# Optimization experiments

Hardware: AMD Instinct MI355X
Metric: run time of the kernel (lower is better)

Reference implementation:

```python
import jax, jax.numpy as jnp
import numpy as np

P, N, F, H, D_HID = 3, 4096, 1024, 8, 8
EMBED = H * D_HID  # 64
ATT, C = 128, 16


def setup_inputs() -> dict:
    key = jax.random.key(0)
    ks = jax.random.split(key, 12)
    return {
        "inputs": jax.random.normal(ks[0], (P, N, F), jnp.float32),
        # bias_mat plays the role of an additive adjacency mask; random floats are fine for math checking
        "bias_mat": jax.random.normal(ks[1], (P, N, N), jnp.float32),
        "W": jax.random.normal(ks[2], (P, H, F, D_HID), jnp.float32) * 0.05,
        "a1_w": jax.random.normal(ks[3], (P, H, D_HID), jnp.float32) * 0.1,
        "a1_b": jax.random.normal(ks[4], (P, H), jnp.float32) * 0.1,
        "a2_w": jax.random.normal(ks[5], (P, H, D_HID), jnp.float32) * 0.1,
        "a2_b": jax.random.normal(ks[6], (P, H), jnp.float32) * 0.1,
        "h_bias": jnp.zeros((P, H, D_HID), jnp.float32),
        "Ws": jax.random.normal(ks[7], (EMBED, ATT), jnp.float32) * 0.1,
        "bs": jax.random.normal(ks[8], (ATT,), jnp.float32) * 0.1,
        "u": jax.random.normal(ks[9], (ATT,), jnp.float32) * 0.1,
        "Wc": jax.random.normal(ks[10], (EMBED, C), jnp.float32) * 0.05,
        "bc": jnp.zeros((C,), jnp.float32),
    }


def reference(inputs, bias_mat, W, a1_w, a1_b, a2_w, a2_b, h_bias, Ws, bs, u, Wc, bc):
    # inputs: [P,N,F], bias_mat: [P,N,N]
    embeds = []
    for p in range(inputs.shape[0]):  # small fixed loop over meta-paths
        seq = inputs[p]                                            # [N,F]
        fts = jnp.einsum('nf,hfd->hnd', seq, W[p])                 # shared projection, all heads
        f1 = jnp.einsum('hnd,hd->hn', fts, a1_w[p]) + a1_b[p][:, None]
        f2 = jnp.einsum('hnd,hd->hn', fts, a2_w[p]) + a2_b[p][:, None]
        logits = f1[:, :, None] + f2[:, None, :]                   # [H,N,N] additive attention
        coefs = jax.nn.softmax(jax.nn.leaky_relu(logits) + bias_mat[p][None], axis=-1)
        vals = jnp.einsum('hnm,hmd->hnd', coefs, fts) + h_bias[p][:, None, :]
        h = jax.nn.elu(vals)                                       # activation per head
        embeds.append(jnp.transpose(h, (1, 0, 2)).reshape(h.shape[1], -1))  # concat heads -> [N,H*d]
    multi = jnp.stack(embeds, axis=1)                              # [N,P,EMBED]
    # semantic (meta-path) attention
    v = jnp.tanh(multi @ Ws + bs)                                  # [N,P,ATT]
    alphas = jax.nn.softmax(v @ u, axis=-1)                        # [N,P]
    final = jnp.sum(multi * alphas[:, :, None], axis=1)            # [N,EMBED]
    # single final classifier head (mean over 1 head == identity)
    logits_out = final @ Wc + bc                                   # [N,C]
    return logits_out, final, alphas
```

## Files before the change

### kernel.cpp

```cpp
#include <hip/hip_runtime.h>

#define LOG2E 1.44269504088896f

typedef _Float16 f16;
typedef _Float16 f16x8 __attribute__((ext_vector_type(8)));
typedef float f32x4 __attribute__((ext_vector_type(4)));

#define NP 3
#define NN 4096
#define FF 1024
#define HH 8
#define DD 8
#define HD 64

#define OFF_F1S   0
#define OFF_F2S   393216
#define OFF_F2MAX 589824
#define OFF_FTST  590080
#define OFF_MULTI 2162944

#define OUT_FINAL 65536
#define OUT_ALPHA 327680

__global__ __launch_bounds__(256) void kA(const float* __restrict__ inp,
                                          const float* __restrict__ W,
                                          const float* __restrict__ a1w,
                                          const float* __restrict__ a1b,
                                          const float* __restrict__ a2w,
                                          const float* __restrict__ a2b,
                                          char* __restrict__ ws) {
    __shared__ float At[32 * 68];
    __shared__ float Bt[32 * 64];
    __shared__ float ftile[64 * 68];
    const int tid = threadIdx.x;
    const int p = blockIdx.y;
    const int n0 = blockIdx.x * 64;

    const int tr = tid >> 4, tc = tid & 15;
    const int r0 = tr * 4, c0 = tc * 4;
    const int sr = tid >> 2, sq = tid & 3;
    const int bc = tid & 63, bkq = tid >> 6;
    const int hB = bc >> 3, dB = bc & 7;

    float acc[4][4] = {};

    for (int kb = 0; kb < 32; ++kb) {
        const float* asrc = inp + ((size_t)p * NN + n0 + sr) * FF + kb * 32 + sq * 8;
        float4 v0 = *(const float4*)asrc;
        float4 v1 = *(const float4*)(asrc + 4);
        int kbase = sq * 8;
        At[(kbase + 0) * 68 + sr] = v0.x; At[(kbase + 1) * 68 + sr] = v0.y;
        At[(kbase + 2) * 68 + sr] = v0.z; At[(kbase + 3) * 68 + sr] = v0.w;
        At[(kbase + 4) * 68 + sr] = v1.x; At[(kbase + 5) * 68 + sr] = v1.y;
        At[(kbase + 6) * 68 + sr] = v1.z; At[(kbase + 7) * 68 + sr] = v1.w;
        #pragma unroll
        for (int i = 0; i < 8; ++i) {
            int k = bkq * 8 + i;
            Bt[k * 64 + bc] = W[(((size_t)p * HH + hB) * FF + kb * 32 + k) * DD + dB];
        }
        __syncthreads();
        #pragma unroll
        for (int k = 0; k < 32; ++k) {
            float4 av = *(const float4*)&At[k * 68 + r0];
            float4 bv = *(const float4*)&Bt[k * 64 + c0];
            float aa[4] = {av.x, av.y, av.z, av.w};
            float bb[4] = {bv.x, bv.y, bv.z, bv.w};
            #pragma unroll
            for (int i = 0; i < 4; ++i)
                #pragma unroll
                for (int j = 0; j < 4; ++j) acc[i][j] += aa[i] * bb[j];
        }
        __syncthreads();
    }
    #pragma unroll
    for (int i = 0; i < 4; ++i) {
        float4 o;
        o.x = acc[i][0]; o.y = acc[i][1]; o.z = acc[i][2]; o.w = acc[i][3];
        *(float4*)&ftile[(r0 + i) * 68 + c0] = o;
    }
    __syncthreads();

    float* f1s = (float*)(ws + OFF_F1S);
    f16* f2s = (f16*)(ws + OFF_F2S);
    #pragma unroll
    for (int rep = 0; rep < 2; ++rep) {
        int task = tid + rep * 256;
        int row = task >> 3, h = task & 7;
        const float* fb = &ftile[row * 68 + h * 8];
        float s1 = a1b[p * HH + h], s2 = a2b[p * HH + h];
        #pragma unroll
        for (int d = 0; d < 8; ++d) {
            float v = fb[d];
            s1 += v * a1w[((size_t)p * HH + h) * DD + d];
            s2 += v * a2w[((size_t)p * HH + h) * DD + d];
        }
        f1s[((size_t)p * HH + h) * NN + n0 + row] = s1 * LOG2E;
        f2s[((size_t)p * HH + h) * NN + n0 + row] = (f16)(s2 * LOG2E);
    }
    {
        f16* ftsT = (f16*)(ws + OFF_FTST);
        int cc2 = tid >> 2, rq = (tid & 3) * 16;
        union { f16 h[16]; uint4 u[2]; } pk;
        #pragma unroll
        for (int i = 0; i < 16; ++i) pk.h[i] = (f16)ftile[(rq + i) * 68 + cc2];
        uint4* dst = (uint4*)(ftsT + ((size_t)p * HD + cc2) * NN + n0 + rq);
        dst[0] = pk.u[0];
        dst[1] = pk.u[1];
    }
}

__global__ __launch_bounds__(64) void kA2(char* __restrict__ ws) {
    const f16* f2s = (const f16*)(ws + OFF_F2S);
    float* fmax = (float*)(ws + OFF_F2MAX);
    int b = blockIdx.x;
    int lane = threadIdx.x;
    float v = -1e30f;
    for (int m = lane; m < NN; m += 64) v = fmaxf(v, (float)f2s[(size_t)b * NN + m]);
    #pragma unroll
    for (int off = 32; off >= 1; off >>= 1) v = fmaxf(v, __shfl_xor(v, off, 64));
    if (lane == 0) fmax[b] = v;
}

__global__ __launch_bounds__(256) void kB(const float* __restrict__ bias,
                                          const float* __restrict__ h_bias,
                                          char* __restrict__ ws) {
    __shared__ __align__(16) char smem[38544];
    f16* ftsL = (f16*)smem;
    f16* f2L = (f16*)(smem + 34320);

    const int tid = threadIdx.x;
    const int lane = tid & 63, wv = tid >> 6;
    const int c = lane & 15, kg = lane >> 4;
    const int p = blockIdx.y;
    const int n0 = blockIdx.x * 16;
    const int n = n0 + c;

    const float* f1s = (const float*)(ws + OFF_F1S);
    const f16* f2s = (const f16*)(ws + OFF_F2S);
    const float* fmax = (const float*)(ws + OFF_F2MAX);
    const f16* ftsG = (const f16*)(ws + OFF_FTST);
    float* multi = (float*)(ws + OFF_MULTI);

    float f18[8], ub[8];
    #pragma unroll
    for (int h = 0; h < 8; ++h) {
        float f1v = f1s[((size_t)p * 8 + h) * NN + n];
        float fm = fmax[p * 8 + h];
        float x = f1v + fm;
        float lr = fmaxf(x, 0.01f * x);
        ub[h] = lr + 8.0f * LOG2E;
        f18[h] = f1v;
    }
    f32x4 acc[8] = {};

    for (int i = tid; i < 264; i += 256) ftsL[64 * 264 + i] = (f16)1.0f;

    const int scc = tid >> 2, sq = tid & 3;
    const int fh = (tid & 127) >> 4, fq = tid & 15;

    for (int ch = 0; ch < 16; ++ch) {
        int m0 = ch * 256;
        {
            const uint4* src = (const uint4*)(ftsG + ((size_t)p * HD + scc) * NN + m0 + sq * 64);
            uint4* dst = (uint4*)(ftsL + scc * 264 + sq * 64);
            #pragma unroll
            for (int i = 0; i < 8; ++i) dst[i] = src[i];
        }
        if (tid < 128) {
            const uint4* src = (const uint4*)(f2s + ((size_t)p * 8 + fh) * NN + m0 + fq * 16);
            uint4* dst = (uint4*)(f2L + fh * 264 + fq * 16);
            dst[0] = src[0];
            dst[1] = src[1];
        }
        __syncthreads();
        #pragma unroll
        for (int s = 0; s < 2; ++s) {
            int mloc = wv * 64 + s * 32 + kg * 8;
            const float* bp = bias + ((size_t)p * NN + n) * NN + m0 + mloc;
            float4 b0 = *(const float4*)bp;
            float4 b1 = *(const float4*)(bp + 4);
            float bb[8] = {b0.x, b0.y, b0.z, b0.w, b1.x, b1.y, b1.z, b1.w};
            #pragma unroll
            for (int h = 0; h < 8; ++h) {
                f16x8 f2v = *(const f16x8*)(f2L + h * 264 + mloc);
                int rB = (c < 8) ? (h * 8 + c) : 64;
                f16x8 bf = *(const f16x8*)(ftsL + rB * 264 + mloc);
                union { f16x8 v; f16 e[8]; } af;
                #pragma unroll
                for (int j = 0; j < 8; ++j) {
                    float x = f18[h] + (float)f2v[j];
                    float lr = fmaxf(x, 0.01f * x);
                    float e = __builtin_amdgcn_exp2f(fmaf(bb[j], LOG2E, lr - ub[h]));
                    af.e[j] = (f16)e;
                }
                acc[h] = __builtin_amdgcn_mfma_f32_16x16x32_f16(af.v, bf, acc[h], 0, 0, 0);
            }
        }
        __syncthreads();
    }

    float* red = (float*)smem;
    #pragma unroll
    for (int h = 0; h < 8; ++h) {
        if (c <= 8) {
            #pragma unroll
            for (int r = 0; r < 4; ++r)
                red[((wv * 8 + h) * 16 + kg * 4 + r) * 9 + c] = acc[h][r];
        }
    }
    __syncthreads();
    #pragma unroll
    for (int rep = 0; rep < 4; ++rep) {
        int idx = tid + rep * 256;
        int R = idx >> 6, hd = idx & 63;
        int h = hd >> 3, d = hd & 7;
        float v = 0.f, l = 0.f;
        #pragma unroll
        for (int w = 0; w < 4; ++w) {
            v += red[((w * 8 + h) * 16 + R) * 9 + d];
            l += red[((w * 8 + h) * 16 + R) * 9 + 8];
        }
        float o = v / l + h_bias[(p * 8 + h) * 8 + d];
        o = o > 0.f ? o : (__builtin_amdgcn_exp2f(o * LOG2E) - 1.0f);
        multi[((size_t)(n0 + R) * NP + p) * HD + hd] = o;
    }
}

__global__ __launch_bounds__(256) void kC(const float* __restrict__ Ws,
                                          const float* __restrict__ bsv,
                                          const float* __restrict__ uv,
                                          const float* __restrict__ Wc,
                                          const float* __restrict__ bcv,
                                          char* __restrict__ ws,
                                          float* __restrict__ out) {
    __shared__ float WsL[64 * 128];
    __shared__ float mult[16 * 3 * 64];
    __shared__ float WcL[64 * 16];
    __shared__ float uL[128], bsL[128], bcL[16];
    __shared__ float vred[16 * 3 * 16];
    __shared__ float alphaL[16 * 3];
    __shared__ float fin[16 * 64];
    const int tid = threadIdx.x;
    const int n0 = blockIdx.x * 16;
    const float* multi = (const float*)(ws + OFF_MULTI);

    for (int i = tid; i < 64 * 128; i += 256) WsL[i] = Ws[i];
    for (int i = tid; i < 3072; i += 256) mult[i] = multi[(size_t)n0 * 192 + i];
    for (int i = tid; i < 1024; i += 256) WcL[i] = Wc[i];
    if (tid < 128) { uL[tid] = uv[tid]; bsL[tid] = bsv[tid]; }
    if (tid < 16) bcL[tid] = bcv[tid];
    __syncthreads();

    const int nl = tid >> 4, j = tid & 15;
    for (int p = 0; p < 3; ++p) {
        float va[8] = {};
        for (int e = 0; e < 64; ++e) {
            float me = mult[(nl * 3 + p) * 64 + e];
            #pragma unroll
            for (int i = 0; i < 8; ++i) va[i] += me * WsL[e * 128 + j + 16 * i];
        }
        float part = 0.f;
        #pragma unroll
        for (int i = 0; i < 8; ++i) part += tanhf(va[i] + bsL[j + 16 * i]) * uL[j + 16 * i];
        vred[(nl * 3 + p) * 16 + j] = part;
    }
    __syncthreads();
    if (tid < 16) {
        float sc[3];
        for (int p = 0; p < 3; ++p) {
            float s = 0.f;
            for (int jj = 0; jj < 16; ++jj) s += vred[(tid * 3 + p) * 16 + jj];
            sc[p] = s;
        }
        float mx = fmaxf(sc[0], fmaxf(sc[1], sc[2]));
        float e0 = __builtin_amdgcn_exp2f((sc[0] - mx) * LOG2E);
        float e1 = __builtin_amdgcn_exp2f((sc[1] - mx) * LOG2E);
        float e2 = __builtin_amdgcn_exp2f((sc[2] - mx) * LOG2E);
        float inv = 1.f / (e0 + e1 + e2);
        float a0 = e0 * inv, a1 = e1 * inv, a2 = e2 * inv;
        alphaL[tid * 3 + 0] = a0; alphaL[tid * 3 + 1] = a1; alphaL[tid * 3 + 2] = a2;
        out[OUT_ALPHA + (size_t)(n0 + tid) * 3 + 0] = a0;
        out[OUT_ALPHA + (size_t)(n0 + tid) * 3 + 1] = a1;
        out[OUT_ALPHA + (size_t)(n0 + tid) * 3 + 2] = a2;
    }
    __syncthreads();
    for (int idx = tid; idx < 1024; idx += 256) {
        int nn2 = idx >> 6, e = idx & 63;
        float f = 0.f;
        for (int p = 0; p < 3; ++p) f += mult[(nn2 * 3 + p) * 64 + e] * alphaL[nn2 * 3 + p];
        fin[nn2 * 64 + e] = f;
        out[OUT_FINAL + (size_t)(n0 + nn2) * 64 + e] = f;
    }
    __syncthreads();
    {
        int nn2 = tid >> 4, cc2 = tid & 15;
        float lg = bcL[cc2];
        for (int e = 0; e < 64; ++e) lg += fin[nn2 * 64 + e] * WcL[e * 16 + cc2];
        out[(size_t)(n0 + nn2) * 16 + cc2] = lg;
    }
}

extern "C" void kernel_launch(void* const* d_in, const int* in_sizes, int n_in,
                              void* d_out, int out_size, void* d_ws, size_t ws_size,
                              hipStream_t stream) {
    (void)in_sizes; (void)n_in; (void)out_size; (void)ws_size;
    const float* inp = (const float*)d_in[0];
    const float* bias = (const float*)d_in[1];
    const float* W = (const float*)d_in[2];
    const float* a1w = (const float*)d_in[3];
    const float* a1b = (const float*)d_in[4];
    const float* a2w = (const float*)d_in[5];
    const float* a2b = (const float*)d_in[6];
    const float* hb = (const float*)d_in[7];
    const float* Wsv = (const float*)d_in[8];
    const float* bsv = (const float*)d_in[9];
    const float* uv = (const float*)d_in[10];
    const float* Wcv = (const float*)d_in[11];
    const float* bcv = (const float*)d_in[12];
    char* ws = (char*)d_ws;
    float* out = (float*)d_out;

    hipLaunchKernelGGL(kA, dim3(64, 3), dim3(256), 0, stream, inp, W, a1w, a1b, a2w, a2b, ws);
    hipLaunchKernelGGL(kA2, dim3(24), dim3(64), 0, stream, ws);
    hipLaunchKernelGGL(kB, dim3(256, 3), dim3(256), 0, stream, bias, hb, ws);
    hipLaunchKernelGGL(kC, dim3(256), dim3(256), 0, stream, Wsv, bsv, uv, Wcv, bcv, ws, out);
}
```

Baseline: 480.0 us.

## Drop LDS staging in attention kernel, read global directly with bias prefetch

The kB kernel no longer stages fts and f2 chunks into shared memory with per-chunk barriers. Each wave now reads them directly from global memory (or L2) over its own contiguous 1024-column slice, and the next bias tile is software-prefetched into registers. The leaky-ReLU and exp-argument arithmetic is also refactored into precomputed per-head constants to cut per-element ALU work. This removes the __syncthreads stalls and LDS traffic, at the cost of redundant global reads of fts/f2 across waves and blocks, which depend on cache hits.

```diff
diff --git a/kernel.cpp b/kernel.cpp
--- a/kernel.cpp
+++ b/kernel.cpp
@@ -124,9 +124,7 @@
 __global__ __launch_bounds__(256) void kB(const float* __restrict__ bias,
                                           const float* __restrict__ h_bias,
                                           char* __restrict__ ws) {
-    __shared__ __align__(16) char smem[38544];
-    f16* ftsL = (f16*)smem;
-    f16* f2L = (f16*)(smem + 34320);
+    __shared__ float red[4 * 8 * 16 * 9];
 
     const int tid = threadIdx.x;
     const int lane = tid & 63, wv = tid >> 6;
@@ -141,65 +139,61 @@
     const f16* ftsG = (const f16*)(ws + OFF_FTST);
     float* multi = (float*)(ws + OFF_MULTI);
 
-    float f18[8], ub[8];
+    float A1[8], B1[8];
     #pragma unroll
     for (int h = 0; h < 8; ++h) {
         float f1v = f1s[((size_t)p * 8 + h) * NN + n];
         float fm = fmax[p * 8 + h];
         float x = f1v + fm;
         float lr = fmaxf(x, 0.01f * x);
-        ub[h] = lr + 8.0f * LOG2E;
-        f18[h] = f1v;
-    }
+        float ub = lr + 8.0f * LOG2E;
+        A1[h] = f1v - ub;
+        B1[h] = fmaf(0.01f, f1v, -ub);
+    }
+
+    union { f16x8 v; unsigned short u[8]; } onesu;
+    #pragma unroll
+    for (int i = 0; i < 8; ++i) onesu.u[i] = 0x3C00;
+    const bool isones = (c >= 8);
+    const int rBc = c & 7;
+
+    const f16* f2base = f2s + (size_t)p * 8 * NN;
+    const f16* ftbase = ftsG + (size_t)p * HD * NN;
+    const float* bbase = bias + ((size_t)p * NN + n) * NN + wv * 1024 + kg * 8;
+
     f32x4 acc[8] = {};
 
-    for (int i = tid; i < 264; i += 256) ftsL[64 * 264 + i] = (f16)1.0f;
-
-    const int scc = tid >> 2, sq = tid & 3;
-    const int fh = (tid & 127) >> 4, fq = tid & 15;
-
-    for (int ch = 0; ch < 16; ++ch) {
-        int m0 = ch * 256;
-        {
-            const uint4* src = (const uint4*)(ftsG + ((size_t)p * HD + scc) * NN + m0 + sq * 64);
-            uint4* dst = (uint4*)(ftsL + scc * 264 + sq * 64);
+    float4 b0 = *(const float4*)(bbase);
+    float4 b1 = *(const float4*)(bbase + 4);
+
+    #pragma unroll 1
+    for (int t = 0; t < 32; ++t) {
+        const int ml = wv * 1024 + t * 32 + kg * 8;
+        const float* bpn = bbase + (((t + 1) & 31) - t) * 32 + t * 32;
+        float4 nb0 = *(const float4*)(bpn);
+        float4 nb1 = *(const float4*)(bpn + 4);
+
+        float bbl[8] = {b0.x * LOG2E, b0.y * LOG2E, b0.z * LOG2E, b0.w * LOG2E,
+                        b1.x * LOG2E, b1.y * LOG2E, b1.z * LOG2E, b1.w * LOG2E};
+
+        #pragma unroll
+        for (int h = 0; h < 8; ++h) {
+            f16x8 f2v = *(const f16x8*)(f2base + (size_t)h * NN + ml);
+            f16x8 bf = *(const f16x8*)(ftbase + (size_t)(h * 8 + rBc) * NN + ml);
+            if (isones) bf = onesu.v;
+            union { f16x8 v; f16 e[8]; } af;
             #pragma unroll
-            for (int i = 0; i < 8; ++i) dst[i] = src[i];
-        }
-        if (tid < 128) {
-            const uint4* src = (const uint4*)(f2s + ((size_t)p * 8 + fh) * NN + m0 + fq * 16);
-            uint4* dst = (uint4*)(f2L + fh * 264 + fq * 16);
-            dst[0] = src[0];
-            dst[1] = src[1];
-        }
-        __syncthreads();
-        #pragma unroll
-        for (int s = 0; s < 2; ++s) {
-            int mloc = wv * 64 + s * 32 + kg * 8;
-            const float* bp = bias + ((size_t)p * NN + n) * NN + m0 + mloc;
-            float4 b0 = *(const float4*)bp;
-            float4 b1 = *(const float4*)(bp + 4);
-            float bb[8] = {b0.x, b0.y, b0.z, b0.w, b1.x, b1.y, b1.z, b1.w};
-            #pragma unroll
-            for (int h = 0; h < 8; ++h) {
-                f16x8 f2v = *(const f16x8*)(f2L + h * 264 + mloc);
-                int rB = (c < 8) ? (h * 8 + c) : 64;
-                f16x8 bf = *(const f16x8*)(ftsL + rB * 264 + mloc);
-                union { f16x8 v; f16 e[8]; } af;
-                #pragma unroll
-                for (int j = 0; j < 8; ++j) {
-                    float x = f18[h] + (float)f2v[j];
-                    float lr = fmaxf(x, 0.01f * x);
-                    float e = __builtin_amdgcn_exp2f(fmaf(bb[j], LOG2E, lr - ub[h]));
-                    af.e[j] = (f16)e;
-                }
-                acc[h] = __builtin_amdgcn_mfma_f32_16x16x32_f16(af.v, bf, acc[h], 0, 0, 0);
+            for (int j = 0; j < 8; ++j) {
+                float f2f = (float)f2v[j];
+                float t1 = f2f + A1[h];
+                float t2 = fmaf(0.01f, f2f, B1[h]);
+                af.e[j] = (f16)__builtin_amdgcn_exp2f(fmaxf(t1, t2) + bbl[j]);
             }
-        }
-        __syncthreads();
-    }
-
-    float* red = (float*)smem;
+            acc[h] = __builtin_amdgcn_mfma_f32_16x16x32_f16(af.v, bf, acc[h], 0, 0, 0);
+        }
+        b0 = nb0; b1 = nb1;
+    }
+
     #pragma unroll
     for (int h = 0; h < 8; ++h) {
         if (c <= 8) {
```

Result: slower. 514.2 us (+7.1%).

## Prefetch bias one chunk ahead and simplify leaky-relu exp arithmetic in kB

Applied to the files above, without the earlier changes.

The bias loads for the next chunk are now issued register-side before the current chunk's compute, so global latency on the dominant N×N bias stream can overlap the MFMA and exp work. The leaky-relu and subtract-max step is rewritten algebraically as max(f2+A1, 0.01*f2+B1), which drops per-element operations. f2 is converted to fp32 once into shared memory so the inner loop skips f16-to-f32 conversions. The fts staging loads are reorganised for coalescing. In exchange the kernel uses more registers and about 4 KB more shared memory, which may reduce occupancy.

```diff
diff --git a/kernel.cpp b/kernel.cpp
--- a/kernel.cpp
+++ b/kernel.cpp
@@ -124,9 +124,9 @@
 __global__ __launch_bounds__(256) void kB(const float* __restrict__ bias,
                                           const float* __restrict__ h_bias,
                                           char* __restrict__ ws) {
-    __shared__ __align__(16) char smem[38544];
+    __shared__ __align__(16) char smem[42768];
     f16* ftsL = (f16*)smem;
-    f16* f2L = (f16*)(smem + 34320);
+    float* f2L = (float*)(smem + 34320);
 
     const int tid = threadIdx.x;
     const int lane = tid & 63, wv = tid >> 6;
@@ -141,62 +141,97 @@
     const f16* ftsG = (const f16*)(ws + OFF_FTST);
     float* multi = (float*)(ws + OFF_MULTI);
 
-    float f18[8], ub[8];
+    float A1[8], B1[8];
     #pragma unroll
     for (int h = 0; h < 8; ++h) {
         float f1v = f1s[((size_t)p * 8 + h) * NN + n];
         float fm = fmax[p * 8 + h];
         float x = f1v + fm;
         float lr = fmaxf(x, 0.01f * x);
-        ub[h] = lr + 8.0f * LOG2E;
-        f18[h] = f1v;
-    }
+        float ub = lr + 8.0f * LOG2E;
+        A1[h] = f1v - ub;
+        B1[h] = fmaf(0.01f, f1v, -ub);
+    }
+
+    for (int i = tid; i < 264; i += 256) ftsL[64 * 264 + i] = (f16)1.0f;
+
+    const int sg = tid >> 3, se = tid & 7;
+    const int srow = sg & 7, sq = sg >> 3;
+    const int f2r = tid >> 5, f2c = (tid & 31) * 8;
+
+    const f16* ftsP = ftsG + (size_t)p * HD * NN;
+    const f16* f2P = f2s + (size_t)p * 8 * NN;
+
+    const int rowsel = (c < 8) ? c * 264 : 64 * 264;
+    const int hstep = (c < 8) ? 8 * 264 : 0;
+
+    const float* bb_base = bias + ((size_t)p * NN + n) * NN + wv * 64 + kg * 8;
+
     f32x4 acc[8] = {};
 
-    for (int i = tid; i < 264; i += 256) ftsL[64 * 264 + i] = (f16)1.0f;
-
-    const int scc = tid >> 2, sq = tid & 3;
-    const int fh = (tid & 127) >> 4, fq = tid & 15;
-
+    float4 uA0 = *(const float4*)(bb_base);
+    float4 uA1 = *(const float4*)(bb_base + 4);
+    float4 uB0 = *(const float4*)(bb_base + 32);
+    float4 uB1 = *(const float4*)(bb_base + 36);
+
+    #pragma unroll 1
     for (int ch = 0; ch < 16; ++ch) {
-        int m0 = ch * 256;
+        const int m0 = ch * 256;
+        const int chn = (ch + 1 < 16) ? ch + 1 : 15;
+        const float* bpn = bb_base + chn * 256;
+        float4 nA0 = *(const float4*)(bpn);
+        float4 nA1 = *(const float4*)(bpn + 4);
+        float4 nB0 = *(const float4*)(bpn + 32);
+        float4 nB1 = *(const float4*)(bpn + 36);
+
         {
-            const uint4* src = (const uint4*)(ftsG + ((size_t)p * HD + scc) * NN + m0 + sq * 64);
-            uint4* dst = (uint4*)(ftsL + scc * 264 + sq * 64);
-            #pragma unroll
-            for (int i = 0; i < 8; ++i) dst[i] = src[i];
-        }
-        if (tid < 128) {
-            const uint4* src = (const uint4*)(f2s + ((size_t)p * 8 + fh) * NN + m0 + fq * 16);
-            uint4* dst = (uint4*)(f2L + fh * 264 + fq * 16);
-            dst[0] = src[0];
-            dst[1] = src[1];
+            const f16* gsrc = ftsP + m0 + sq * 64 + se * 8;
+            f16* ldst = ftsL + srow * 264 + sq * 64 + se * 8;
+            #pragma unroll
+            for (int k = 0; k < 8; ++k) {
+                *(uint4*)(ldst + k * 8 * 264) =
+                    *(const uint4*)(gsrc + (size_t)(srow + k * 8) * NN);
+            }
+        }
+        {
+            union { uint4 u; f16 h[8]; } t16;
+            t16.u = *(const uint4*)(f2P + (size_t)f2r * NN + m0 + f2c);
+            float4 lo, hi;
+            lo.x = (float)t16.h[0]; lo.y = (float)t16.h[1];
+            lo.z = (float)t16.h[2]; lo.w = (float)t16.h[3];
+            hi.x = (float)t16.h[4]; hi.y = (float)t16.h[5];
+            hi.z = (float)t16.h[6]; hi.w = (float)t16.h[7];
+            *(float4*)(f2L + f2r * 264 + f2c) = lo;
+            *(float4*)(f2L + f2r * 264 + f2c + 4) = hi;
         }
         __syncthreads();
+
         #pragma unroll
         for (int s = 0; s < 2; ++s) {
-            int mloc = wv * 64 + s * 32 + kg * 8;
-            const float* bp = bias + ((size_t)p * NN + n) * NN + m0 + mloc;
-            float4 b0 = *(const float4*)bp;
-            float4 b1 = *(const float4*)(bp + 4);
-            float bb[8] = {b0.x, b0.y, b0.z, b0.w, b1.x, b1.y, b1.z, b1.w};
+            const int mloc = wv * 64 + s * 32 + kg * 8;
+            float4 bv0 = s ? uB0 : uA0;
+            float4 bv1 = s ? uB1 : uA1;
+            float bbl[8] = {bv0.x * LOG2E, bv0.y * LOG2E, bv0.z * LOG2E, bv0.w * LOG2E,
+                            bv1.x * LOG2E, bv1.y * LOG2E, bv1.z * LOG2E, bv1.w * LOG2E};
             #pragma unroll
             for (int h = 0; h < 8; ++h) {
-                f16x8 f2v = *(const f16x8*)(f2L + h * 264 + mloc);
-                int rB = (c < 8) ? (h * 8 + c) : 64;
-                f16x8 bf = *(const f16x8*)(ftsL + rB * 264 + mloc);
+                const float* f2p = f2L + h * 264 + mloc;
+                float4 f2a = *(const float4*)f2p;
+                float4 f2b = *(const float4*)(f2p + 4);
+                float f2arr[8] = {f2a.x, f2a.y, f2a.z, f2a.w, f2b.x, f2b.y, f2b.z, f2b.w};
+                f16x8 bf = *(const f16x8*)(ftsL + rowsel + h * hstep + mloc);
                 union { f16x8 v; f16 e[8]; } af;
                 #pragma unroll
                 for (int j = 0; j < 8; ++j) {
-                    float x = f18[h] + (float)f2v[j];
-                    float lr = fmaxf(x, 0.01f * x);
-                    float e = __builtin_amdgcn_exp2f(fmaf(bb[j], LOG2E, lr - ub[h]));
-                    af.e[j] = (f16)e;
+                    float t1 = f2arr[j] + A1[h];
+                    float t2 = fmaf(0.01f, f2arr[j], B1[h]);
+                    af.e[j] = (f16)__builtin_amdgcn_exp2f(fmaxf(t1, t2) + bbl[j]);
                 }
                 acc[h] = __builtin_amdgcn_mfma_f32_16x16x32_f16(af.v, bf, acc[h], 0, 0, 0);
             }
         }
         __syncthreads();
+        uA0 = nA0; uA1 = nA1; uB0 = nB0; uB1 = nB1;
     }
 
     float* red = (float*)smem;
```

After: 467.9 us. 1.03x faster.
